# Performance work log

Measured on AMD Instinct MI355X. Metric: run time of the kernel, lower is better.

## Reference

```python
import jax, jax.numpy as jnp
import numpy as np


def setup_inputs() -> dict:
    key = jax.random.key(0)
    ks = jax.random.split(key, 8)
    B, S, Ta, D = 64, 512, 8, 768
    return {
        "memory": jax.random.normal(ks[0], (B, S, D), dtype=jnp.float32),
        "aspect_states": jax.random.normal(ks[1], (B, Ta, D), dtype=jnp.float32),
        "input_ids": jnp.ones((B, S), dtype=jnp.int64),
        "input_t_ids": jnp.ones((B, Ta), dtype=jnp.int64),
        "W1": jax.random.normal(ks[2], (3 * D, D), dtype=jnp.float32) * 0.02,
        "b1": jnp.zeros((D,), dtype=jnp.float32),
        "w2": jax.random.normal(ks[3], (D,), dtype=jnp.float32) * 0.02,
        "Wm": jax.random.normal(ks[4], (D, D), dtype=jnp.float32) * 0.02,
        "bm": jnp.zeros((D,), dtype=jnp.float32),
        "Wd": jax.random.normal(ks[5], (D, 3), dtype=jnp.float32) * 0.02,
        "bd": jnp.zeros((3,), dtype=jnp.float32),
    }


def reference(memory, aspect_states, input_ids, input_t_ids, W1, b1, w2, Wm, bm, Wd, bd):
    B, S, D = memory.shape
    memory_len = jnp.sum(input_ids != 0, axis=-1)          # [B]
    aspect_len = jnp.sum(input_t_ids != 0, axis=-1)        # [B]

    # v_a: mean-pooled aspect representation  [B, D]
    v_a = jnp.sum(aspect_states, axis=1) / aspect_len.astype(memory.dtype)[:, None]
    # v_s: mean-pooled sentence representation [B, D]
    v_s = jnp.sum(memory, axis=1) / memory_len.astype(memory.dtype)[:, None]

    # locationed_memory: memory[i, idx] *= 1 - idx/memory_len[i] for idx < memory_len[i]
    idx = jnp.arange(S, dtype=memory.dtype)                 # [S]
    mlen = memory_len.astype(memory.dtype)[:, None]         # [B, 1]
    loc = jnp.where(idx[None, :] < mlen, 1.0 - idx[None, :] / mlen, 1.0)  # [B, S]
    memory = memory * loc[:, :, None]

    # chunked linear1/linear2 scorer, vectorized:
    # c_t = w2 . tanh(W1 @ [m_t ; v_a ; v_s] + b1)
    W1_m, W1_a, W1_s = W1[:D], W1[D:2 * D], W1[2 * D:]
    ctx = v_a @ W1_a + v_s @ W1_s + b1                      # [B, D]
    h = jnp.tanh(jnp.einsum("bsd,de->bse", memory, W1_m) + ctx[:, None, :])
    scores = h @ w2                                         # [B, S]
    alpha = jax.nn.softmax(scores, axis=1)

    v_ts = jnp.einsum("bsd,bs->bd", memory, alpha)          # [B, D]
    v_ns = v_ts + v_s
    v_ms = jnp.tanh(v_ns @ Wm + bm)
    logits = v_ms @ Wd + bd                                 # [B, 3]
    return logits
```

## Files before the change

kernel.cpp:

```cpp
#include <hip/hip_runtime.h>
#include <hip/hip_bf16.h>


#define NB 64
#define NS 512
#define ND 768
#define NTA 8

typedef __attribute__((ext_vector_type(8))) __bf16 bf16x8;
typedef __attribute__((ext_vector_type(4))) float f32x4;

#define OFF_SCORES 0u
#define OFF_VS 131072u
#define OFF_VTS 327680u
#define OFF_CTX 524288u
#define OFF_U 720896u
#define ZERO_BYTES 917504u
#define OFF_VA 917504u
#define OFF_LENS 1114112u
#define OFF_W1MT 1115136u
#define OFF_MP 2294784u

__device__ __forceinline__ float fast_tanh(float x) {
  x = fminf(fmaxf(x, -15.f), 15.f);
  float t = __expf(2.f * x);
  return __fdividef(t - 1.f, t + 1.f);
}

__device__ __forceinline__ unsigned bfpack2(float a, float b) {
  unsigned ua = __float_as_uint(a), ub = __float_as_uint(b);
  ua = (ua + 0x7FFFu + ((ua >> 16) & 1u)) >> 16;
  ub = (ub + 0x7FFFu + ((ub >> 16) & 1u)) >> 16;
  return ua | (ub << 16);
}

__device__ __forceinline__ unsigned short bf16b(float f) {
  unsigned u = __float_as_uint(f);
  u = (u + 0x7FFFu + ((u >> 16) & 1u)) >> 16;
  return (unsigned short)u;
}

__device__ __forceinline__ void async_copy16(const void* g, void* l) {
  __builtin_amdgcn_global_load_lds(
      (const __attribute__((address_space(1))) void*)g,
      (__attribute__((address_space(3))) void*)l, 16, 0, 0);
}

__global__ __launch_bounds__(256) void k_prep_tr(const int* __restrict__ ids,
                                                 const int* __restrict__ tids,
                                                 const float* __restrict__ aspect,
                                                 const float* __restrict__ W1,
                                                 float* __restrict__ v_a,
                                                 float* __restrict__ lens,
                                                 unsigned short* __restrict__ w1mt) {
  int bid = blockIdx.x, tid = threadIdx.x;
  if (bid < 576) {
    __shared__ float tile[32][33];
    int bx = bid % 24, by = bid / 24;
    int tx = tid & 31, ty = tid >> 5;
    for (int j = 0; j < 32; j += 8)
      tile[ty + j][tx] = W1[(size_t)(by * 32 + ty + j) * ND + bx * 32 + tx];
    __syncthreads();
    for (int j = 0; j < 32; j += 8)
      w1mt[(size_t)(bx * 32 + ty + j) * ND + by * 32 + tx] = bf16b(tile[tx][ty + j]);
  } else {
    int b = bid - 576;
    __shared__ int red[256];
    __shared__ float sh_inva;
    int cnt = 0;
    for (int j = tid; j < NS; j += 256) cnt += (ids[b * NS + j] != 0);
    red[tid] = cnt;
    __syncthreads();
    for (int s = 128; s > 0; s >>= 1) {
      if (tid < s) red[tid] += red[tid + s];
      __syncthreads();
    }
    if (tid == 0) {
      int mlen = red[0];
      int acnt = 0;
      for (int t = 0; t < NTA; ++t) acnt += (tids[b * NTA + t] != 0);
      lens[b] = (float)mlen;
      lens[64 + b] = 1.0f / (float)mlen;
      float inva = 1.0f / (float)acnt;
      lens[128 + b] = inva;
      sh_inva = inva;
    }
    __syncthreads();
    float inva = sh_inva;
    for (int j = tid; j < ND; j += 256) {
      float s = 0.f;
      for (int t = 0; t < NTA; ++t) s += aspect[((size_t)b * NTA + t) * ND + j];
      v_a[b * ND + j] = s * inva;
    }
  }
}

__global__ __launch_bounds__(192) void k_vs_mprime(const float* __restrict__ memory,
                                                   const float* __restrict__ lens,
                                                   float* __restrict__ v_s,
                                                   unsigned short* __restrict__ mp) {
  int sc = blockIdx.x, b = blockIdx.y, tid = threadIdx.x;
  int d0 = tid * 4;
  float inv_mlen = lens[64 + b];
  float mlenf = lens[b];
  float s0 = 0, s1 = 0, s2 = 0, s3 = 0;
#pragma unroll 8
  for (int s = 0; s < 32; ++s) {
    int srow = sc * 32 + s;
    size_t row = (size_t)b * NS + srow;
    const float4 v = *(const float4*)(memory + row * ND + d0);
    s0 += v.x; s1 += v.y; s2 += v.z; s3 += v.w;
    float fs = (float)srow;
    float loc = (fs < mlenf) ? 1.0f - fs * inv_mlen : 1.0f;
    uint2 pk;
    pk.x = bfpack2(v.x * loc, v.y * loc);
    pk.y = bfpack2(v.z * loc, v.w * loc);
    *(uint2*)(mp + row * ND + d0) = pk;
  }
  float* p = v_s + b * ND + d0;
  atomicAdd(p + 0, s0 * inv_mlen);
  atomicAdd(p + 1, s1 * inv_mlen);
  atomicAdd(p + 2, s2 * inv_mlen);
  atomicAdd(p + 3, s3 * inv_mlen);
}

__global__ __launch_bounds__(128) void k_ctx(const float* __restrict__ W1,
                                             const float* __restrict__ v_a,
                                             const float* __restrict__ v_s,
                                             float* __restrict__ ctx) {
  int b = blockIdx.x, et = blockIdx.y, dc = blockIdx.z, tid = threadIdx.x;
  __shared__ float vbuf[384];
  for (int j = tid; j < 384; j += 128) {
    int k = dc * 384 + j;
    vbuf[j] = (k < ND) ? v_a[b * ND + k] : v_s[b * ND + (k - ND)];
  }
  __syncthreads();
  int e = et * 128 + tid;
  float acc = 0.f;
  const float* Wk = W1 + (size_t)(ND + dc * 384) * ND + e;
#pragma unroll 8
  for (int j = 0; j < 384; ++j) acc += vbuf[j] * Wk[(size_t)j * ND];
  atomicAdd(&ctx[b * ND + e], acc);
}

__global__ __launch_bounds__(256) void k_gemm_scores(const unsigned short* __restrict__ mp,
                                                     const unsigned short* __restrict__ w1mt,
                                                     const float* __restrict__ ctx,
                                                     const float* __restrict__ b1,
                                                     const float* __restrict__ w2,
                                                     float* __restrict__ scores) {
  __shared__ char lds[65536];
  const int tid = threadIdx.x;
  const int wave = tid >> 6, lane = tid & 63;
  const int bid = blockIdx.x;
  const int swz = (bid & 7) * 192 + (bid >> 3);
  const int rt = swz / 6;
  const int et = swz - rt * 6;
  const int row0 = rt * 128, n0 = et * 128;
  const int b = row0 >> 9;
  const int wm = wave & 1, wn = wave >> 1;

  const int lrow = lane >> 3;
  const int qlog = (lane & 7) ^ lrow;
  const char* Abase = (const char*)mp + (size_t)(row0 + lrow) * (ND * 2) + qlog * 16;
  const char* Bbase = (const char*)w1mt + (size_t)(n0 + lrow) * (ND * 2) + qlog * 16;

  f32x4 acc[4][4];
#pragma unroll
  for (int i = 0; i < 4; ++i)
#pragma unroll
    for (int t = 0; t < 4; ++t) acc[i][t] = (f32x4){0.f, 0.f, 0.f, 0.f};

  const int q2 = lane >> 4, c = lane & 15;
  int offA[4][2], offB[4][2];
#pragma unroll
  for (int i = 0; i < 4; ++i) {
    int ml = wm * 64 + i * 16 + c;
    offA[i][0] = ml * 128 + ((q2 ^ (ml & 7)) * 16);
    offA[i][1] = ml * 128 + (((4 + q2) ^ (ml & 7)) * 16);
    int nl = wn * 64 + i * 16 + c;
    offB[i][0] = nl * 128 + ((q2 ^ (nl & 7)) * 16);
    offB[i][1] = nl * 128 + (((4 + q2) ^ (nl & 7)) * 16);
  }

  auto stage = [&](int bufsel, int kb) {
    char* lA = lds + bufsel * 32768;
    char* lB = lA + 16384;
#pragma unroll
    for (int i = 0; i < 4; ++i) {
      int g = wave * 4 + i;
      async_copy16(Abase + (size_t)g * 8 * (ND * 2) + kb, lA + g * 1024);
      async_copy16(Bbase + (size_t)g * 8 * (ND * 2) + kb, lB + g * 1024);
    }
  };

  stage(0, 0);
  stage(1, 128);

#pragma unroll
  for (int t = 0; t < 12; ++t) {
    if (t < 11) { asm volatile("s_waitcnt vmcnt(8)" ::: "memory"); }
    else        { asm volatile("s_waitcnt vmcnt(0)" ::: "memory"); }
    __builtin_amdgcn_s_barrier();
    __builtin_amdgcn_sched_barrier(0);
    const char* lA = lds + (t & 1) * 32768;
    const char* lB = lA + 16384;
    bf16x8 af[2][4], bfr[2][4];
#pragma unroll
    for (int kk = 0; kk < 2; ++kk)
#pragma unroll
      for (int i = 0; i < 4; ++i) {
        af[kk][i] = *(const bf16x8*)(lA + offA[i][kk]);
        bfr[kk][i] = *(const bf16x8*)(lB + offB[i][kk]);
      }
    __builtin_amdgcn_s_setprio(1);
#pragma unroll
    for (int kk = 0; kk < 2; ++kk)
#pragma unroll
      for (int i = 0; i < 4; ++i)
#pragma unroll
        for (int t2 = 0; t2 < 4; ++t2)
          acc[i][t2] = __builtin_amdgcn_mfma_f32_16x16x32_bf16(af[kk][i], bfr[kk][t2], acc[i][t2], 0, 0, 0);
    __builtin_amdgcn_s_setprio(0);
    asm volatile("s_waitcnt lgkmcnt(0)" ::: "memory");
    __builtin_amdgcn_s_barrier();
    __builtin_amdgcn_sched_barrier(0);
    if (t + 2 < 12) stage(t & 1, (t + 2) * 128);
  }

  float ctxv[4], w2v[4];
#pragma unroll
  for (int t = 0; t < 4; ++t) {
    int n = n0 + wn * 64 + t * 16 + c;
    ctxv[t] = ctx[b * ND + n] + b1[n];
    w2v[t] = w2[n];
  }
#pragma unroll
  for (int i = 0; i < 4; ++i) {
#pragma unroll
    for (int r = 0; r < 4; ++r) {
      float s = 0.f;
#pragma unroll
      for (int t = 0; t < 4; ++t) s += fast_tanh(acc[i][t][r] + ctxv[t]) * w2v[t];
      s += __shfl_xor(s, 1, 64);
      s += __shfl_xor(s, 2, 64);
      s += __shfl_xor(s, 4, 64);
      s += __shfl_xor(s, 8, 64);
      if (c == 0) atomicAdd(&scores[row0 + wm * 64 + i * 16 + q2 * 4 + r], s);
    }
  }
}

__global__ __launch_bounds__(192) void k_vts(const unsigned short* __restrict__ mp,
                                             const float* __restrict__ scores,
                                             float* __restrict__ v_ts) {
  int sc = blockIdx.x, b = blockIdx.y, tid = threadIdx.x;
  int lane = tid & 63, wid = tid >> 6;
  __shared__ float sred[3], sred2[3];
  __shared__ float al[32];
  float v0 = scores[b * NS + tid];
  float v1 = scores[b * NS + tid + 192];
  float v2 = (tid < 128) ? scores[b * NS + tid + 384] : -1e30f;
  float m = fmaxf(fmaxf(v0, v1), v2);
  for (int off = 1; off < 64; off <<= 1) m = fmaxf(m, __shfl_xor(m, off, 64));
  if (lane == 0) sred[wid] = m;
  __syncthreads();
  float M = fmaxf(fmaxf(sred[0], sred[1]), sred[2]);
  float e = __expf(v0 - M) + __expf(v1 - M) + ((tid < 128) ? __expf(v2 - M) : 0.f);
  for (int off = 1; off < 64; off <<= 1) e += __shfl_xor(e, off, 64);
  if (lane == 0) sred2[wid] = e;
  __syncthreads();
  float invS = 1.0f / (sred2[0] + sred2[1] + sred2[2]);
  if (tid < 32) al[tid] = __expf(scores[b * NS + sc * 32 + tid] - M) * invS;
  __syncthreads();

  int d0 = tid * 4;
  float a0 = 0, a1 = 0, a2 = 0, a3 = 0;
#pragma unroll 4
  for (int s = 0; s < 32; ++s) {
    size_t row = (size_t)b * NS + sc * 32 + s;
    uint2 pk = *(const uint2*)(mp + row * ND + d0);
    float a = al[s];
    a0 += a * __uint_as_float(pk.x << 16);
    a1 += a * __uint_as_float(pk.x & 0xFFFF0000u);
    a2 += a * __uint_as_float(pk.y << 16);
    a3 += a * __uint_as_float(pk.y & 0xFFFF0000u);
  }
  float* p = v_ts + b * ND + d0;
  atomicAdd(p + 0, a0);
  atomicAdd(p + 1, a1);
  atomicAdd(p + 2, a2);
  atomicAdd(p + 3, a3);
}

__global__ __launch_bounds__(128) void k_final1(const float* __restrict__ v_ts,
                                                const float* __restrict__ v_s,
                                                const float* __restrict__ Wm,
                                                float* __restrict__ u) {
  int b = blockIdx.x, et = blockIdx.y, dc = blockIdx.z, tid = threadIdx.x;
  __shared__ float vbuf[192];
  for (int j = tid; j < 192; j += 128) {
    int d = dc * 192 + j;
    vbuf[j] = v_ts[b * ND + d] + v_s[b * ND + d];
  }
  __syncthreads();
  int e = et * 128 + tid;
  float acc = 0.f;
  const float* Wk = Wm + (size_t)(dc * 192) * ND + e;
#pragma unroll 8
  for (int j = 0; j < 192; ++j) acc += vbuf[j] * Wk[(size_t)j * ND];
  atomicAdd(&u[b * ND + e], acc);
}

__global__ __launch_bounds__(256) void k_final2(const float* __restrict__ u,
                                                const float* __restrict__ bm,
                                                const float* __restrict__ Wd,
                                                const float* __restrict__ bd,
                                                float* __restrict__ out) {
  int b = blockIdx.x, tid = threadIdx.x;
  int wid = tid >> 6, lane = tid & 63;
  __shared__ float red[4][3];
  float p0 = 0, p1 = 0, p2 = 0;
  for (int e = tid; e < ND; e += 256) {
    float vm = fast_tanh(u[b * ND + e] + bm[e]);
    p0 += vm * Wd[e * 3 + 0];
    p1 += vm * Wd[e * 3 + 1];
    p2 += vm * Wd[e * 3 + 2];
  }
  for (int off = 1; off < 64; off <<= 1) {
    p0 += __shfl_xor(p0, off, 64);
    p1 += __shfl_xor(p1, off, 64);
    p2 += __shfl_xor(p2, off, 64);
  }
  if (lane == 0) { red[wid][0] = p0; red[wid][1] = p1; red[wid][2] = p2; }
  __syncthreads();
  if (tid == 0) {
    out[b * 3 + 0] = red[0][0] + red[1][0] + red[2][0] + red[3][0] + bd[0];
    out[b * 3 + 1] = red[0][1] + red[1][1] + red[2][1] + red[3][1] + bd[1];
    out[b * 3 + 2] = red[0][2] + red[1][2] + red[2][2] + red[3][2] + bd[2];
  }
}

extern "C" void kernel_launch(void* const* d_in, const int* in_sizes, int n_in,
                              void* d_out, int out_size, void* d_ws, size_t ws_size,
                              hipStream_t stream) {
  const float* memory = (const float*)d_in[0];
  const float* aspect = (const float*)d_in[1];
  const int* ids = (const int*)d_in[2];
  const int* tids = (const int*)d_in[3];
  const float* W1 = (const float*)d_in[4];
  const float* b1 = (const float*)d_in[5];
  const float* w2 = (const float*)d_in[6];
  const float* Wm = (const float*)d_in[7];
  const float* bm = (const float*)d_in[8];
  const float* Wd = (const float*)d_in[9];
  const float* bd = (const float*)d_in[10];
  float* out = (float*)d_out;

  char* ws = (char*)d_ws;
  float* scores = (float*)(ws + OFF_SCORES);
  float* v_s = (float*)(ws + OFF_VS);
  float* v_ts = (float*)(ws + OFF_VTS);
  float* ctx = (float*)(ws + OFF_CTX);
  float* u = (float*)(ws + OFF_U);
  float* v_a = (float*)(ws + OFF_VA);
  float* lens = (float*)(ws + OFF_LENS);
  unsigned short* w1mt = (unsigned short*)(ws + OFF_W1MT);
  unsigned short* mp = (unsigned short*)(ws + OFF_MP);

  hipMemsetAsync(ws, 0, ZERO_BYTES, stream);

  k_prep_tr<<<640, 256, 0, stream>>>(ids, tids, aspect, W1, v_a, lens, w1mt);
  k_vs_mprime<<<dim3(16, NB), 192, 0, stream>>>(memory, lens, v_s, mp);
  k_ctx<<<dim3(64, 6, 4), 128, 0, stream>>>(W1, v_a, v_s, ctx);
  k_gemm_scores<<<1536, 256, 0, stream>>>(mp, w1mt, ctx, b1, w2, scores);
  k_vts<<<dim3(16, NB), 192, 0, stream>>>(mp, scores, v_ts);
  k_final1<<<dim3(64, 6, 4), 128, 0, stream>>>(v_ts, v_s, Wm, u);
  k_final2<<<NB, 256, 0, stream>>>(u, bm, Wd, bd, out);
}
```

Baseline: 303.8 us.

## Widen per-thread vectors in mprime/weighted-sum kernels and simplify GEMM double-buffer pipeline

Result: slower. 367.5 us (+21.0%).

```diff
diff --git a/kernel.cpp b/kernel.cpp
--- a/kernel.cpp
+++ b/kernel.cpp
@@ -100,28 +100,38 @@
                                                    float* __restrict__ v_s,
                                                    unsigned short* __restrict__ mp) {
   int sc = blockIdx.x, b = blockIdx.y, tid = threadIdx.x;
-  int d0 = tid * 4;
+  int dq = tid % 96, half = tid / 96;
+  int d0 = dq * 8;
   float inv_mlen = lens[64 + b];
   float mlenf = lens[b];
-  float s0 = 0, s1 = 0, s2 = 0, s3 = 0;
-#pragma unroll 8
-  for (int s = 0; s < 32; ++s) {
-    int srow = sc * 32 + s;
+  float s0 = 0, s1 = 0, s2 = 0, s3 = 0, s4 = 0, s5 = 0, s6 = 0, s7 = 0;
+  int sbase = sc * 32 + half * 16;
+#pragma unroll 4
+  for (int s = 0; s < 16; ++s) {
+    int srow = sbase + s;
     size_t row = (size_t)b * NS + srow;
-    const float4 v = *(const float4*)(memory + row * ND + d0);
-    s0 += v.x; s1 += v.y; s2 += v.z; s3 += v.w;
+    const float4 va = *(const float4*)(memory + row * ND + d0);
+    const float4 vb = *(const float4*)(memory + row * ND + d0 + 4);
+    s0 += va.x; s1 += va.y; s2 += va.z; s3 += va.w;
+    s4 += vb.x; s5 += vb.y; s6 += vb.z; s7 += vb.w;
     float fs = (float)srow;
     float loc = (fs < mlenf) ? 1.0f - fs * inv_mlen : 1.0f;
-    uint2 pk;
-    pk.x = bfpack2(v.x * loc, v.y * loc);
-    pk.y = bfpack2(v.z * loc, v.w * loc);
-    *(uint2*)(mp + row * ND + d0) = pk;
+    uint4 pk;
+    pk.x = bfpack2(va.x * loc, va.y * loc);
+    pk.y = bfpack2(va.z * loc, va.w * loc);
+    pk.z = bfpack2(vb.x * loc, vb.y * loc);
+    pk.w = bfpack2(vb.z * loc, vb.w * loc);
+    *(uint4*)(mp + row * ND + d0) = pk;
   }
   float* p = v_s + b * ND + d0;
   atomicAdd(p + 0, s0 * inv_mlen);
   atomicAdd(p + 1, s1 * inv_mlen);
   atomicAdd(p + 2, s2 * inv_mlen);
   atomicAdd(p + 3, s3 * inv_mlen);
+  atomicAdd(p + 4, s4 * inv_mlen);
+  atomicAdd(p + 5, s5 * inv_mlen);
+  atomicAdd(p + 6, s6 * inv_mlen);
+  atomicAdd(p + 7, s7 * inv_mlen);
 }
 
 __global__ __launch_bounds__(128) void k_ctx(const float* __restrict__ W1,
@@ -195,15 +205,13 @@
   };
 
   stage(0, 0);
-  stage(1, 128);
-
-#pragma unroll
+  __syncthreads();
+
+  int cur = 0;
+#pragma unroll 2
   for (int t = 0; t < 12; ++t) {
-    if (t < 11) { asm volatile("s_waitcnt vmcnt(8)" ::: "memory"); }
-    else        { asm volatile("s_waitcnt vmcnt(0)" ::: "memory"); }
-    __builtin_amdgcn_s_barrier();
-    __builtin_amdgcn_sched_barrier(0);
-    const char* lA = lds + (t & 1) * 32768;
+    if (t < 11) stage(cur ^ 1, (t + 1) * 128);
+    const char* lA = lds + cur * 32768;
     const char* lB = lA + 16384;
     bf16x8 af[2][4], bfr[2][4];
 #pragma unroll
@@ -213,7 +221,6 @@
         af[kk][i] = *(const bf16x8*)(lA + offA[i][kk]);
         bfr[kk][i] = *(const bf16x8*)(lB + offB[i][kk]);
       }
-    __builtin_amdgcn_s_setprio(1);
 #pragma unroll
     for (int kk = 0; kk < 2; ++kk)
 #pragma unroll
@@ -221,11 +228,8 @@
 #pragma unroll
         for (int t2 = 0; t2 < 4; ++t2)
           acc[i][t2] = __builtin_amdgcn_mfma_f32_16x16x32_bf16(af[kk][i], bfr[kk][t2], acc[i][t2], 0, 0, 0);
-    __builtin_amdgcn_s_setprio(0);
-    asm volatile("s_waitcnt lgkmcnt(0)" ::: "memory");
-    __builtin_amdgcn_s_barrier();
-    __builtin_amdgcn_sched_barrier(0);
-    if (t + 2 < 12) stage(t & 1, (t + 2) * 128);
+    __syncthreads();
+    cur ^= 1;
   }
 
   float ctxv[4], w2v[4];
@@ -274,23 +278,33 @@
   if (tid < 32) al[tid] = __expf(scores[b * NS + sc * 32 + tid] - M) * invS;
   __syncthreads();
 
-  int d0 = tid * 4;
-  float a0 = 0, a1 = 0, a2 = 0, a3 = 0;
+  int dq = tid % 96, half = tid / 96;
+  int d0 = dq * 8;
+  float a0 = 0, a1 = 0, a2 = 0, a3 = 0, a4 = 0, a5 = 0, a6 = 0, a7 = 0;
+  int sbase = half * 16;
 #pragma unroll 4
-  for (int s = 0; s < 32; ++s) {
-    size_t row = (size_t)b * NS + sc * 32 + s;
-    uint2 pk = *(const uint2*)(mp + row * ND + d0);
-    float a = al[s];
+  for (int s = 0; s < 16; ++s) {
+    size_t row = (size_t)b * NS + sc * 32 + sbase + s;
+    uint4 pk = *(const uint4*)(mp + row * ND + d0);
+    float a = al[sbase + s];
     a0 += a * __uint_as_float(pk.x << 16);
     a1 += a * __uint_as_float(pk.x & 0xFFFF0000u);
     a2 += a * __uint_as_float(pk.y << 16);
     a3 += a * __uint_as_float(pk.y & 0xFFFF0000u);
+    a4 += a * __uint_as_float(pk.z << 16);
+    a5 += a * __uint_as_float(pk.z & 0xFFFF0000u);
+    a6 += a * __uint_as_float(pk.w << 16);
+    a7 += a * __uint_as_float(pk.w & 0xFFFF0000u);
   }
   float* p = v_ts + b * ND + d0;
   atomicAdd(p + 0, a0);
   atomicAdd(p + 1, a1);
   atomicAdd(p + 2, a2);
   atomicAdd(p + 3, a3);
+  atomicAdd(p + 4, a4);
+  atomicAdd(p + 5, a5);
+  atomicAdd(p + 6, a6);
+  atomicAdd(p + 7, a7);
 }
 
 __global__ __launch_bounds__(128) void k_final1(const float* __restrict__ v_ts,
```
